# Performance work log

Measured on AMD Instinct MI355X. Metric: run time of the kernel, lower is better.

The kernel has to match this reference:

```python
import jax, jax.numpy as jnp
import numpy as np

N = 1024      # side of the square relation matrix
K = 64        # in_dim
OUT = 64      # out_dim
N_W = 15      # h_params_asym


def setup_inputs() -> dict:
    key = jax.random.key(0)
    k1, k2 = jax.random.split(key)
    S = N * N
    input_layer = jax.random.normal(k1, (S, K), dtype=jnp.float32)
    stdv = 1.0 / float(np.sqrt(K))
    weights = jax.random.uniform(k2, (N_W, K, OUT), minval=-stdv, maxval=stdv, dtype=jnp.float32)
    ar = jnp.arange(S, dtype=jnp.int32)
    rows = ar // N                       # row index of each flattened entry
    cols = ar % N                        # col index of each flattened entry
    idx_trans = cols * N + rows          # transpose permutation
    idx_diag = jnp.arange(N, dtype=jnp.int32) * (N + 1)  # diagonal positions
    idx_all = jnp.zeros((S,), dtype=jnp.int32)           # single segment
    idx_diag_broad = jnp.zeros((N,), dtype=jnp.int32)    # pool diag to one segment
    col_norm = jnp.full((N,), float(N), dtype=jnp.float32)   # each column-segment has N members
    row_norm = jnp.full((N,), float(N), dtype=jnp.float32)
    all_norm = jnp.array([float(S)], dtype=jnp.float32)
    diag_norm = jnp.array([float(N)], dtype=jnp.float32)
    return dict(input_layer=input_layer, weights=weights,
                idx_trans=idx_trans, idx_diag=idx_diag, idx_row=rows, idx_col=cols,
                idx_all=idx_all, idx_diag_broad=idx_diag_broad,
                col_norm=col_norm, row_norm=row_norm, all_norm=all_norm, diag_norm=diag_norm)


def reference(input_layer, weights, idx_trans, idx_diag, idx_row, idx_col,
              idx_all, idx_diag_broad, col_norm, row_norm, all_norm, diag_norm):
    S = input_layer.shape[0]
    n = idx_diag.shape[0]
    out_dim = weights.shape[2]

    def pool(X, idx, norm, nseg):
        # normalized segment mean (index_add then divide)
        return jax.ops.segment_sum(X, idx, num_segments=nseg) / norm[:, None]

    def scatter_diag(X):
        # scatter n rows onto the diagonal positions of an [S, out_dim] zero tensor
        return jnp.zeros((S, out_dim), X.dtype).at[idx_diag].set(X)

    transpose = input_layer[idx_trans]            # [S, k]
    diagonal = input_layer[idx_diag]              # [n, k]
    row_pool = pool(input_layer, idx_col, col_norm, n)   # [n, k]
    col_pool = pool(input_layer, idx_row, row_norm, n)   # [n, k]
    all_pool = pool(input_layer, idx_all, all_norm, 1)   # [1, k]
    diag_pool = pool(diagonal, idx_diag_broad, diag_norm, 1)  # [1, k]

    output = input_layer @ weights[0]
    output += transpose @ weights[1]
    output += scatter_diag(diagonal @ weights[2])
    output += (row_pool @ weights[3])[idx_col]    # row_pool broadcast over col idx
    output += (row_pool @ weights[4])[idx_row]    # row_pool broadcast over row idx
    output += (col_pool @ weights[5])[idx_row]
    output += (col_pool @ weights[6])[idx_col]
    output += (all_pool @ weights[7])[idx_all]
    output += scatter_diag((diag_pool @ weights[8])[idx_diag_broad])
    output += scatter_diag((all_pool @ weights[9])[idx_diag_broad])
    output += scatter_diag(row_pool @ weights[10])
    output += scatter_diag(col_pool @ weights[11])
    output += (diag_pool @ weights[12])[idx_all]
    output += (diagonal @ weights[13])[idx_col]
    output += (diagonal @ weights[14])[idx_row]
    return output
```

## Files before the change

### kernel.cpp

```cpp
#include <hip/hip_runtime.h>
#include <hip/hip_bf16.h>

typedef __attribute__((ext_vector_type(4))) short shortx4;
typedef __attribute__((ext_vector_type(8))) short short8;
typedef __attribute__((ext_vector_type(4))) float floatx4;

__device__ __forceinline__ unsigned short f2bf(float f) {
    __hip_bfloat16 h = __float2bfloat16(f);
    return __builtin_bit_cast(unsigned short, h);
}

#define GLOAD_LDS16(g, l) __builtin_amdgcn_global_load_lds(                      \
    (const __attribute__((address_space(1))) void*)(g),                          \
    (__attribute__((address_space(3))) void*)(l), 16, 0, 0)

__global__ __launch_bounds__(256) void sweep_kernel(const float* __restrict__ in,
        unsigned short* __restrict__ bfcopy, float* __restrict__ rowpart,
        float* __restrict__ colpart, float* __restrict__ diagbuf) {
    __shared__ float colp[4][16][64];
    int t = threadIdx.x;
    int kq = t & 15;
    int cl = (t >> 4) & 3;
    int w  = t >> 6;
    int c  = w * 4 + cl;
    int ti = blockIdx.y, tj = blockIdx.x;
    int R = ti * 16, C = tj * 16;
    const float* base = in + ((size_t)R << 16) + (size_t)(C + c) * 64 + kq * 4;
    unsigned short* tbase = bfcopy + ((size_t)(ti * 64 + tj) << 14);
    bool dt = (ti == tj);

    floatx4 rowacc = (floatx4){0.f, 0.f, 0.f, 0.f};
    #pragma unroll
    for (int i = 0; i < 16; ++i) {
        floatx4 v = __builtin_nontemporal_load((const floatx4*)(base + ((size_t)i << 16)));
        rowacc += v;
        int row = i * 16 + c;
        int wg = (kq >> 1) ^ ((row ^ (row >> 4)) & 7);
        shortx4 h;
        h[0] = (short)f2bf(v[0]); h[1] = (short)f2bf(v[1]);
        h[2] = (short)f2bf(v[2]); h[3] = (short)f2bf(v[3]);
        *(shortx4*)(tbase + (size_t)row * 64 + wg * 8 + (kq & 1) * 4) = h;
        if (dt && c == i)
            *(floatx4*)&diagbuf[(size_t)(R + i) * 64 + kq * 4] = v;
        floatx4 cs = v;
        #pragma unroll
        for (int m = 16; m <= 32; m <<= 1) {
            cs[0] += __shfl_xor(cs[0], m);
            cs[1] += __shfl_xor(cs[1], m);
            cs[2] += __shfl_xor(cs[2], m);
            cs[3] += __shfl_xor(cs[3], m);
        }
        if (cl == 0) *(floatx4*)&colp[w][i][kq * 4] = cs;
    }
    *(floatx4*)&rowpart[(size_t)ti * 65536 + (size_t)(C + c) * 64 + kq * 4] = rowacc;
    __syncthreads();
    int i2 = t >> 4, kq2 = t & 15;
    floatx4 s = *(const floatx4*)&colp[0][i2][kq2 * 4];
    s += *(const floatx4*)&colp[1][i2][kq2 * 4];
    s += *(const floatx4*)&colp[2][i2][kq2 * 4];
    s += *(const floatx4*)&colp[3][i2][kq2 * 4];
    *(floatx4*)&colpart[(size_t)tj * 65536 + (size_t)(R + i2) * 64 + kq2 * 4] = s;
}

__global__ __launch_bounds__(256) void poolfin_kernel(const float* __restrict__ rowpart,
        const float* __restrict__ colpart, const float* __restrict__ diagbuf,
        const float* __restrict__ wts,
        float* __restrict__ row_pool, float* __restrict__ col_pool,
        float* __restrict__ allraw, float* __restrict__ diagraw,
        unsigned short* __restrict__ w0t, unsigned short* __restrict__ w1t) {
    __shared__ float red[16][64];
    int b = blockIdx.x, t = threadIdx.x;
    if (b < 64) {
        int j = b * 256 + t;
        const floatx4* rp4 = (const floatx4*)rowpart;
        floatx4 s = (floatx4){0.f, 0.f, 0.f, 0.f};
        #pragma unroll 8
        for (int y = 0; y < 64; ++y) s += rp4[(size_t)y * 16384 + j];
        *(floatx4*)&row_pool[j * 4] = s * (1.f / 1024.f);
    } else if (b < 128) {
        int j = (b - 64) * 256 + t;
        const floatx4* cp4 = (const floatx4*)colpart;
        floatx4 s = (floatx4){0.f, 0.f, 0.f, 0.f};
        #pragma unroll 8
        for (int y = 0; y < 64; ++y) s += cp4[(size_t)y * 16384 + j];
        *(floatx4*)&col_pool[j * 4] = s * (1.f / 1024.f);
        *(floatx4*)&red[t >> 4][(t & 15) * 4] = s;
        __syncthreads();
        if (t < 64) {
            float a = 0.f;
            #pragma unroll
            for (int q = 0; q < 16; ++q) a += red[q][t];
            atomicAdd(&allraw[t], a);
        }
    } else if (b < 136) {
        int d = b - 128;
        int k = t & 63, rl = t >> 6;
        float sd = 0.f;
        #pragma unroll 8
        for (int u = 0; u < 32; ++u)
            sd += diagbuf[(size_t)(d * 128 + rl + 4 * u) * 64 + k];
        red[rl][k] = sd;
        __syncthreads();
        if (t < 64)
            atomicAdd(&diagraw[t], red[0][t] + red[1][t] + red[2][t] + red[3][t]);
    } else {
        int idx = (b - 136) * 256 + t;
        int n = idx >> 6, k = idx & 63;
        w0t[idx] = f2bf(wts[k * 64 + n]);
        w1t[idx] = f2bf(wts[4096 + k * 64 + n]);
    }
}

__global__ __launch_bounds__(256) void abd_kernel(const float* __restrict__ W,
        const float* __restrict__ col_pool, const float* __restrict__ row_pool,
        const float* __restrict__ diagbuf, const float* __restrict__ allraw,
        const float* __restrict__ diagraw,
        float* __restrict__ Ab, float* __restrict__ Bb, float* __restrict__ Dgb) {
    __shared__ float rp[8][64], cp[8][64], dv[8][64], ap[64], dp[64];
    int t = threadIdx.x, o = t & 63, il = t >> 6;
    int i0 = blockIdx.x * 8;
    #pragma unroll
    for (int q = 0; q < 2; ++q) {
        int ii = il + 4 * q;
        rp[ii][o] = row_pool[(i0 + ii) * 64 + o];
        cp[ii][o] = col_pool[(i0 + ii) * 64 + o];
        dv[ii][o] = diagbuf[(i0 + ii) * 64 + o];
    }
    if (t < 64) {
        ap[t] = allraw[t] * (1.f / 1048576.f);
        dp[t] = diagraw[t] * (1.f / 1024.f);
    }
    __syncthreads();
    int iA = il, iB = il + 4;
    float aA0 = 0.f, aA1 = 0.f, aB0 = 0.f, aB1 = 0.f, aD0 = 0.f, aD1 = 0.f;
    float cA = 0.f, cD = 0.f;
    #pragma unroll 4
    for (int k = 0; k < 64; ++k) {
        int ko = k * 64 + o;
        float w2  = W[2 * 4096 + ko],  w3  = W[3 * 4096 + ko];
        float w4  = W[4 * 4096 + ko],  w5  = W[5 * 4096 + ko];
        float w6  = W[6 * 4096 + ko],  w7  = W[7 * 4096 + ko];
        float w8  = W[8 * 4096 + ko],  w9  = W[9 * 4096 + ko];
        float w10 = W[10 * 4096 + ko], w11 = W[11 * 4096 + ko];
        float w12 = W[12 * 4096 + ko], w13 = W[13 * 4096 + ko];
        float w14 = W[14 * 4096 + ko];
        float rA = rp[iA][k], cAk = cp[iA][k], dA = dv[iA][k];
        float rB = rp[iB][k], cBk = cp[iB][k], dB = dv[iB][k];
        aA0 += rA * w3 + cAk * w6 + dA * w13;
        aA1 += rB * w3 + cBk * w6 + dB * w13;
        aB0 += rA * w4 + cAk * w5 + dA * w14;
        aB1 += rB * w4 + cBk * w5 + dB * w14;
        aD0 += dA * w2 + rA * w10 + cAk * w11;
        aD1 += dB * w2 + rB * w10 + cBk * w11;
        cA += ap[k] * w7 + dp[k] * w12;
        cD += dp[k] * w8 + ap[k] * w9;
    }
    Ab[(i0 + iA) * 64 + o]  = aA0 + cA;
    Ab[(i0 + iB) * 64 + o]  = aA1 + cA;
    Bb[(i0 + iA) * 64 + o]  = aB0;
    Bb[(i0 + iB) * 64 + o]  = aB1;
    Dgb[(i0 + iA) * 64 + o] = aD0 + cD;
    Dgb[(i0 + iB) * 64 + o] = aD1 + cD;
}

__global__ __launch_bounds__(256, 2) void main_kernel(const unsigned short* __restrict__ bfcopy,
        const unsigned short* __restrict__ w0t, const unsigned short* __restrict__ w1t,
        const float* __restrict__ Ab, const float* __restrict__ Bb,
        const float* __restrict__ Dgb, float* __restrict__ out) {
    __shared__ short lds[32768];

    int t = threadIdx.x;
    int lane = t & 63, w = t >> 6;
    int lrow = lane & 15, lhi = lane >> 4;

    int p = blockIdx.x;
    float fb = (129.0f - sqrtf(129.0f * 129.0f - 8.0f * (float)p)) * 0.5f;
    int bi = (int)fb;
    while (bi > 0 && bi * (129 - bi) / 2 > p) --bi;
    while ((bi + 1) * (129 - (bi + 1)) / 2 <= p) ++bi;
    int bj = bi + (p - bi * (129 - bi) / 2);
    int r0 = bi * 16, c0 = bj * 16;
    bool diag = (bi == bj);

    const unsigned short* t0 = bfcopy + ((size_t)(bi * 64 + bj) << 14);
    const unsigned short* t1 = bfcopy + ((size_t)(bj * 64 + bi) << 14);
    #pragma unroll
    for (int n = 0; n < 8; ++n) {
        int g = n * 256 + t;
        GLOAD_LDS16(t0 + g * 8, lds + g * 8);
    }
    if (!diag) {
        #pragma unroll
        for (int n = 0; n < 8; ++n) {
            int g = n * 256 + t;
            GLOAD_LDS16(t1 + g * 8, lds + 16384 + g * 8);
        }
    }

    short8 bw0[2][4], bw1[2][4];
    #pragma unroll
    for (int kg = 0; kg < 2; ++kg)
        #pragma unroll
        for (int nt = 0; nt < 4; ++nt) {
            int off = (nt * 16 + lrow) * 64 + kg * 32 + lhi * 8;
            bw0[kg][nt] = *(const short8*)(w0t + off);
            bw1[kg][nt] = *(const short8*)(w1t + off);
        }
    __syncthreads();

    int base1 = diag ? 0 : 16384;

    #pragma unroll
    for (int sel = 0; sel < 2; ++sel) {
        if (sel == 1 && diag) continue;
        int selb = sel ? base1 : 0;
        int othb = sel ? 0 : base1;
        int rbase = sel ? c0 : r0;
        int cbase = sel ? r0 : c0;
        #pragma unroll
        for (int mf = 0; mf < 4; ++mf) {
            int I = w * 4 + mf;
            int mrow = I * 16 + lrow;
            int swzm = (mrow ^ (mrow >> 4)) & 7;
            int trow = lrow * 16 + I;
            int swzt = (trow ^ (trow >> 4)) & 7;
            short8 ad[2], at2[2];
            #pragma unroll
            for (int kg = 0; kg < 2; ++kg) {
                ad[kg]  = *(const short8*)(lds + selb + mrow * 64 + ((kg * 4 + lhi) ^ swzm) * 8);
                at2[kg] = *(const short8*)(lds + othb + trow * 64 + ((kg * 4 + lhi) ^ swzt) * 8);
            }
            floatx4 acc[4];
            #pragma unroll
            for (int nt = 0; nt < 4; ++nt) acc[nt] = (floatx4){0.f, 0.f, 0.f, 0.f};
            #pragma unroll
            for (int nt = 0; nt < 4; ++nt) {
                acc[nt] = __builtin_amdgcn_mfma_f32_16x16x32_bf16(ad[0],  bw0[0][nt], acc[nt], 0, 0, 0);
                acc[nt] = __builtin_amdgcn_mfma_f32_16x16x32_bf16(ad[1],  bw0[1][nt], acc[nt], 0, 0, 0);
                acc[nt] = __builtin_amdgcn_mfma_f32_16x16x32_bf16(at2[0], bw1[0][nt], acc[nt], 0, 0, 0);
                acc[nt] = __builtin_amdgcn_mfma_f32_16x16x32_bf16(at2[1], bw1[1][nt], acc[nt], 0, 0, 0);
            }
            int ridx = rbase + I;
            float br[4];
            #pragma unroll
            for (int nt = 0; nt < 4; ++nt) br[nt] = Bb[ridx * 64 + nt * 16 + lrow];
            #pragma unroll
            for (int jj = 0; jj < 4; ++jj) {
                int j = lhi * 4 + jj;
                int cidx = cbase + j;
                size_t s = ((size_t)ridx << 10) + cidx;
                bool isd = (ridx == cidx);
                #pragma unroll
                for (int nt = 0; nt < 4; ++nt) {
                    int n = nt * 16 + lrow;
                    float v = acc[nt][jj] + Ab[cidx * 64 + n] + br[nt];
                    if (isd) v += Dgb[ridx * 64 + n];
                    __builtin_nontemporal_store(v, &out[s * 64 + n]);
                }
            }
        }
    }
}

extern "C" void kernel_launch(void* const* d_in, const int* in_sizes, int n_in,
                              void* d_out, int out_size, void* d_ws, size_t ws_size,
                              hipStream_t stream) {
    const float* in  = (const float*)d_in[0];
    const float* wts = (const float*)d_in[1];
    float* out = (float*)d_out;
    float* ws = (float*)d_ws;

    unsigned short* bfcopy = (unsigned short*)ws;
    float* rowpart  = ws + 33554432;
    float* colpart  = ws + 37748736;
    float* row_pool = ws + 41943040;
    float* col_pool = ws + 42008576;
    float* diagbuf  = ws + 42074112;
    float* allraw   = ws + 42139648;
    float* diagraw  = ws + 42139712;
    float* Ab       = ws + 42139776;
    float* Bb       = ws + 42205312;
    float* Dgb      = ws + 42270848;
    unsigned short* w0t = (unsigned short*)(ws + 42336384);
    unsigned short* w1t = w0t + 4096;

    (void)hipMemsetAsync((void*)allraw, 0, 128 * sizeof(float), stream);

    sweep_kernel<<<dim3(64, 64), 256, 0, stream>>>(in, bfcopy, rowpart, colpart, diagbuf);
    poolfin_kernel<<<152, 256, 0, stream>>>(rowpart, colpart, diagbuf, wts,
                                            row_pool, col_pool, allraw, diagraw, w0t, w1t);
    abd_kernel<<<128, 256, 0, stream>>>(wts, col_pool, row_pool, diagbuf,
                                        allraw, diagraw, Ab, Bb, Dgb);
    main_kernel<<<2080, 256, 0, stream>>>(bfcopy, w0t, w1t, Ab, Bb, Dgb, out);
}
```

Before: 215.7 us.

## Shrink main kernel tiles from 16x16 to 8x8 block pairs with matching bf16 layout

The sweep kernel now writes the bf16 copy as 8x8 position tiles (64 rows of 64 features) with a new XOR swizzle. The main kernel processes 8x8 tile pairs (8256 blocks instead of 2080) with a quarter of the LDS, and launch bounds are raised to allow 4 blocks per CU. The goal is more parallelism, better occupancy and a smaller tail. The cost is more blocks, and weight fragments are reloaded per block, so each block does less work to amortize that setup.

New measurement: 238.9 us. 1.11x slower.

```diff
diff --git a/kernel.cpp b/kernel.cpp
--- a/kernel.cpp
+++ b/kernel.cpp
@@ -26,7 +26,6 @@
     int ti = blockIdx.y, tj = blockIdx.x;
     int R = ti * 16, C = tj * 16;
     const float* base = in + ((size_t)R << 16) + (size_t)(C + c) * 64 + kq * 4;
-    unsigned short* tbase = bfcopy + ((size_t)(ti * 64 + tj) << 14);
     bool dt = (ti == tj);
 
     floatx4 rowacc = (floatx4){0.f, 0.f, 0.f, 0.f};
@@ -34,12 +33,13 @@
     for (int i = 0; i < 16; ++i) {
         floatx4 v = __builtin_nontemporal_load((const floatx4*)(base + ((size_t)i << 16)));
         rowacc += v;
-        int row = i * 16 + c;
-        int wg = (kq >> 1) ^ ((row ^ (row >> 4)) & 7);
+        int row64 = (i & 7) * 8 + (c & 7);
+        int tid8 = (ti * 2 + (i >> 3)) * 128 + (tj * 2 + (c >> 3));
+        int wg = (kq >> 1) ^ (row64 & 7) ^ ((row64 >> 3) & 7);
         shortx4 h;
         h[0] = (short)f2bf(v[0]); h[1] = (short)f2bf(v[1]);
         h[2] = (short)f2bf(v[2]); h[3] = (short)f2bf(v[3]);
-        *(shortx4*)(tbase + (size_t)row * 64 + wg * 8 + (kq & 1) * 4) = h;
+        *(shortx4*)(bfcopy + ((size_t)tid8 << 12) + row64 * 64 + wg * 8 + (kq & 1) * 4) = h;
         if (dt && c == i)
             *(floatx4*)&diagbuf[(size_t)(R + i) * 64 + kq * 4] = v;
         floatx4 cs = v;
@@ -163,37 +163,37 @@
     Dgb[(i0 + iB) * 64 + o] = aD1 + cD;
 }
 
-__global__ __launch_bounds__(256, 2) void main_kernel(const unsigned short* __restrict__ bfcopy,
+__global__ __launch_bounds__(256, 4) void main_kernel(const unsigned short* __restrict__ bfcopy,
         const unsigned short* __restrict__ w0t, const unsigned short* __restrict__ w1t,
         const float* __restrict__ Ab, const float* __restrict__ Bb,
         const float* __restrict__ Dgb, float* __restrict__ out) {
-    __shared__ short lds[32768];
+    __shared__ short lds[8192];
 
     int t = threadIdx.x;
     int lane = t & 63, w = t >> 6;
     int lrow = lane & 15, lhi = lane >> 4;
 
     int p = blockIdx.x;
-    float fb = (129.0f - sqrtf(129.0f * 129.0f - 8.0f * (float)p)) * 0.5f;
+    float fb = (257.0f - sqrtf(257.0f * 257.0f - 8.0f * (float)p)) * 0.5f;
     int bi = (int)fb;
-    while (bi > 0 && bi * (129 - bi) / 2 > p) --bi;
-    while ((bi + 1) * (129 - (bi + 1)) / 2 <= p) ++bi;
-    int bj = bi + (p - bi * (129 - bi) / 2);
-    int r0 = bi * 16, c0 = bj * 16;
+    while (bi > 0 && bi * (257 - bi) / 2 > p) --bi;
+    while ((bi + 1) * (257 - (bi + 1)) / 2 <= p) ++bi;
+    int bj = bi + (p - bi * (257 - bi) / 2);
+    int r0 = bi * 8, c0 = bj * 8;
     bool diag = (bi == bj);
 
-    const unsigned short* t0 = bfcopy + ((size_t)(bi * 64 + bj) << 14);
-    const unsigned short* t1 = bfcopy + ((size_t)(bj * 64 + bi) << 14);
-    #pragma unroll
-    for (int n = 0; n < 8; ++n) {
+    const unsigned short* t0 = bfcopy + ((size_t)(bi * 128 + bj) << 12);
+    const unsigned short* t1 = bfcopy + ((size_t)(bj * 128 + bi) << 12);
+    #pragma unroll
+    for (int n = 0; n < 2; ++n) {
         int g = n * 256 + t;
         GLOAD_LDS16(t0 + g * 8, lds + g * 8);
     }
     if (!diag) {
         #pragma unroll
-        for (int n = 0; n < 8; ++n) {
+        for (int n = 0; n < 2; ++n) {
             int g = n * 256 + t;
-            GLOAD_LDS16(t1 + g * 8, lds + 16384 + g * 8);
+            GLOAD_LDS16(t1 + g * 8, lds + 4096 + g * 8);
         }
     }
 
@@ -208,7 +208,12 @@
         }
     __syncthreads();
 
-    int base1 = diag ? 0 : 16384;
+    int base1 = diag ? 0 : 4096;
+
+    int mrow = w * 16 + lrow;
+    int swzm = (mrow & 7) ^ ((mrow >> 3) & 7);
+    int trow = (lrow & 7) * 8 + w * 2 + (lrow >> 3);
+    int swzt = (trow & 7) ^ ((trow >> 3) & 7);
 
     #pragma unroll
     for (int sel = 0; sel < 2; ++sel) {
@@ -217,46 +222,36 @@
         int othb = sel ? 0 : base1;
         int rbase = sel ? c0 : r0;
         int cbase = sel ? r0 : c0;
-        #pragma unroll
-        for (int mf = 0; mf < 4; ++mf) {
-            int I = w * 4 + mf;
-            int mrow = I * 16 + lrow;
-            int swzm = (mrow ^ (mrow >> 4)) & 7;
-            int trow = lrow * 16 + I;
-            int swzt = (trow ^ (trow >> 4)) & 7;
-            short8 ad[2], at2[2];
-            #pragma unroll
-            for (int kg = 0; kg < 2; ++kg) {
-                ad[kg]  = *(const short8*)(lds + selb + mrow * 64 + ((kg * 4 + lhi) ^ swzm) * 8);
-                at2[kg] = *(const short8*)(lds + othb + trow * 64 + ((kg * 4 + lhi) ^ swzt) * 8);
-            }
-            floatx4 acc[4];
-            #pragma unroll
-            for (int nt = 0; nt < 4; ++nt) acc[nt] = (floatx4){0.f, 0.f, 0.f, 0.f};
+
+        short8 ad[2], at2[2];
+        #pragma unroll
+        for (int kg = 0; kg < 2; ++kg) {
+            ad[kg]  = *(const short8*)(lds + selb + mrow * 64 + ((kg * 4 + lhi) ^ swzm) * 8);
+            at2[kg] = *(const short8*)(lds + othb + trow * 64 + ((kg * 4 + lhi) ^ swzt) * 8);
+        }
+        floatx4 acc[4];
+        #pragma unroll
+        for (int nt = 0; nt < 4; ++nt) acc[nt] = (floatx4){0.f, 0.f, 0.f, 0.f};
+        #pragma unroll
+        for (int nt = 0; nt < 4; ++nt) {
+            acc[nt] = __builtin_amdgcn_mfma_f32_16x16x32_bf16(ad[0],  bw0[0][nt], acc[nt], 0, 0, 0);
+            acc[nt] = __builtin_amdgcn_mfma_f32_16x16x32_bf16(ad[1],  bw0[1][nt], acc[nt], 0, 0, 0);
+            acc[nt] = __builtin_amdgcn_mfma_f32_16x16x32_bf16(at2[0], bw1[0][nt], acc[nt], 0, 0, 0);
+            acc[nt] = __builtin_amdgcn_mfma_f32_16x16x32_bf16(at2[1], bw1[1][nt], acc[nt], 0, 0, 0);
+        }
+        #pragma unroll
+        for (int jj = 0; jj < 4; ++jj) {
+            int rl = w * 16 + lhi * 4 + jj;
+            int ridx = rbase + (rl >> 3);
+            int cidx = cbase + (rl & 7);
+            size_t s = ((size_t)ridx << 10) + cidx;
+            bool isd = diag && ((rl >> 3) == (rl & 7));
             #pragma unroll
             for (int nt = 0; nt < 4; ++nt) {
-                acc[nt] = __builtin_amdgcn_mfma_f32_16x16x32_bf16(ad[0],  bw0[0][nt], acc[nt], 0, 0, 0);
-                acc[nt] = __builtin_amdgcn_mfma_f32_16x16x32_bf16(ad[1],  bw0[1][nt], acc[nt], 0, 0, 0);
-                acc[nt] = __builtin_amdgcn_mfma_f32_16x16x32_bf16(at2[0], bw1[0][nt], acc[nt], 0, 0, 0);
-                acc[nt] = __builtin_amdgcn_mfma_f32_16x16x32_bf16(at2[1], bw1[1][nt], acc[nt], 0, 0, 0);
-            }
-            int ridx = rbase + I;
-            float br[4];
-            #pragma unroll
-            for (int nt = 0; nt < 4; ++nt) br[nt] = Bb[ridx * 64 + nt * 16 + lrow];
-            #pragma unroll
-            for (int jj = 0; jj < 4; ++jj) {
-                int j = lhi * 4 + jj;
-                int cidx = cbase + j;
-                size_t s = ((size_t)ridx << 10) + cidx;
-                bool isd = (ridx == cidx);
-                #pragma unroll
-                for (int nt = 0; nt < 4; ++nt) {
-                    int n = nt * 16 + lrow;
-                    float v = acc[nt][jj] + Ab[cidx * 64 + n] + br[nt];
-                    if (isd) v += Dgb[ridx * 64 + n];
-                    __builtin_nontemporal_store(v, &out[s * 64 + n]);
-                }
+                int n = nt * 16 + lrow;
+                float v = acc[nt][jj] + Ab[cidx * 64 + n] + Bb[ridx * 64 + n];
+                if (isd) v += Dgb[ridx * 64 + n];
+                __builtin_nontemporal_store(v, &out[s * 64 + n]);
             }
         }
     }
@@ -291,5 +286,5 @@
                                             row_pool, col_pool, allraw, diagraw, w0t, w1t);
     abd_kernel<<<128, 256, 0, stream>>>(wts, col_pool, row_pool, diagbuf,
                                         allraw, diagraw, Ab, Bb, Dgb);
-    main_kernel<<<2080, 256, 0, stream>>>(bfcopy, w0t, w1t, Ab, Bb, Dgb, out);
-}
+    main_kernel<<<8256, 256, 0, stream>>>(bfcopy, w0t, w1t, Ab, Bb, Dgb, out);
+}
```
